# Performance work log

Hardware: AMD Instinct MI355X
Metric: run time of the kernel (lower is better)

## Reference

```python
import math
import jax, jax.numpy as jnp
import numpy as np

B, N, G, D = 8, 1000, 1000, 2
E, H = 128, 8           # embedding_dim, n_heads
DH = E // H             # head dim
KNN = 16                # n_decoding_neighbors (static: mask all zeros -> K=min(16,N))
TANH_CLIP = 10.0


def make_heads(x, n_heads):
    # (B, n, E) -> (B, n_heads, n, E//n_heads)
    b, n, e = x.shape
    return x.reshape(b, n, n_heads, e // n_heads).transpose(0, 2, 1, 3)


def setup_inputs() -> dict:
    key = jax.random.key(0)
    ks = jax.random.split(key, 12)
    s = 1.0 / math.sqrt(E)
    return {
        "last_node": jax.random.randint(ks[0], (B, G), 0, N),
        "coordinates": jax.random.uniform(ks[1], (B, N, D), dtype=jnp.float32),
        "embeddings": jax.random.normal(ks[2], (B, N, E), dtype=jnp.float32),
        "group_ninf_mask": jnp.zeros((B, G, N), dtype=jnp.float32),
        "Wq_graph": jax.random.normal(ks[3], (E, E), dtype=jnp.float32) * s,
        "Wq_first": jax.random.normal(ks[4], (E, E), dtype=jnp.float32) * s,
        "Wq_last": jax.random.normal(ks[5], (E, E), dtype=jnp.float32) * s,
        "Wk": jax.random.normal(ks[6], (E, E), dtype=jnp.float32) * s,
        "Wv": jax.random.normal(ks[7], (E, E), dtype=jnp.float32) * s,
        "W_comb": jax.random.normal(ks[8], (E, E), dtype=jnp.float32) * s,
        "b_comb": jax.random.normal(ks[9], (E,), dtype=jnp.float32) * s,
    }


def reference(last_node, coordinates, embeddings, group_ninf_mask,
              Wq_graph, Wq_first, Wq_last, Wk, Wv, W_comb, b_comb):
    # --- reset() precomputation ---
    graph_emb = embeddings.mean(axis=1, keepdims=True)          # (B,1,E)
    q_graph = make_heads(graph_emb @ Wq_graph.T, H)             # (B,H,1,DH)
    k_h = make_heads(embeddings @ Wk.T, H)                      # (B,H,N,DH)
    v_h = make_heads(embeddings @ Wv.T, H)                      # (B,H,N,DH)

    # --- gather last node embedding ---
    idx_e = jnp.broadcast_to(last_node[..., None], (B, G, E))
    last_emb = jnp.take_along_axis(embeddings, idx_e, axis=1)   # (B,G,E)
    q_first = make_heads(last_emb @ Wq_first.T, H)              # (B,H,G,DH)
    q_last = make_heads(last_emb @ Wq_last.T, H)
    glimpse_q = q_graph + q_first + q_last                      # (B,H,G,DH)

    # --- KNN neighbor mask (cdist + topk + scatter) ---
    idx_c = jnp.broadcast_to(last_node[..., None], (B, G, D))
    last_coord = jnp.take_along_axis(coordinates, idx_c, axis=1)  # (B,G,D)
    d2 = (jnp.sum(last_coord**2, -1)[:, :, None]
          + jnp.sum(coordinates**2, -1)[:, None, :]
          - 2.0 * jnp.einsum('bgd,bnd->bgn', last_coord, coordinates))
    dist = jnp.sqrt(jnp.maximum(d2, 0.0))                       # (B,G,N)
    dist = jnp.where(group_ninf_mask == -jnp.inf, jnp.inf, dist)
    _, knn_idx = jax.lax.top_k(-dist, KNN)                      # (B,G,K) smallest dists
    bi = jnp.arange(B)[:, None, None]
    gi = jnp.arange(G)[None, :, None]
    glimpse_mask = jnp.full((B, G, N), -jnp.inf, dtype=jnp.float32)
    glimpse_mask = glimpse_mask.at[bi, gi, knn_idx].set(0.0)

    # --- masked multi-head glimpse attention ---
    scores = jnp.einsum('bhgd,bhnd->bhgn', glimpse_q, k_h) / math.sqrt(DH)
    scores = scores + glimpse_mask[:, None, :, :]
    attn = jax.nn.softmax(scores, axis=-1)
    out = jnp.einsum('bhgn,bhnd->bhgd', attn, v_h)              # (B,H,G,DH)
    out = out.transpose(0, 2, 1, 3).reshape(B, G, E)
    final_q = out @ W_comb.T + b_comb                           # (B,G,E)

    # --- tanh-clipped scoring + softmax ---
    score = jnp.einsum('bge,bne->bgn', final_q, embeddings) / math.sqrt(E)
    score_masked = TANH_CLIP * jnp.tanh(score) + group_ninf_mask
    probs = jax.nn.softmax(score_masked, axis=2)                # (B,G,N)
    return probs
```

## Files before the change

### kernel.cpp

```cpp
#include <hip/hip_runtime.h>
#include <math.h>

#define BD 8
#define NN 1000
#define GG 1000
#define EE 128

#define OFF_QG    0
#define OFF_K     1024
#define OFF_V     (OFF_K + 1024000)
#define OFF_QFL   (OFF_V + 1024000)
#define OFF_OUTG  (OFF_QFL + 1024000)
#define OFF_FQ    (OFF_OUTG + 1024000)
#define OFF_PART  (OFF_FQ + 1024000)

__global__ __launch_bounds__(1024) void k_graphq(const float* __restrict__ emb,
                                                 const float* __restrict__ Wqg,
                                                 float* __restrict__ qg) {
  __shared__ float partial[8][128];
  __shared__ float ge[128];
  int b = blockIdx.x;
  int t = threadIdx.x;
  int e = t & 127, p = t >> 7;
  const float* eb = emb + (size_t)b * NN * EE;
  float s = 0.f;
  int n0 = p * 125;
  for (int n = n0; n < n0 + 125; ++n) s += eb[(size_t)n * EE + e];
  partial[p][e] = s;
  __syncthreads();
  if (t < 128) {
    float m = 0.f;
#pragma unroll
    for (int q = 0; q < 8; ++q) m += partial[q][t];
    ge[t] = m * (1.f / 1000.f);
  }
  __syncthreads();
  if (t < 128) {
    const float* wr = Wqg + (size_t)t * EE;
    float acc = 0.f;
#pragma unroll 8
    for (int k = 0; k < 128; ++k) acc += ge[k] * wr[k];
    qg[b * EE + t] = acc;
  }
}

__global__ __launch_bounds__(256) void k_proj(const float* __restrict__ emb,
                                              const float* __restrict__ Wk,
                                              const float* __restrict__ Wv,
                                              const float* __restrict__ Wqf,
                                              const float* __restrict__ Wql,
                                              float* __restrict__ Karr,
                                              float* __restrict__ Varr,
                                              float* __restrict__ QFL) {
  __shared__ float Als[16][68];
  __shared__ float Bls[16][68];
  int mt = blockIdx.x, nt = blockIdx.y;
  int t = threadIdx.x;
  int ty = t >> 4, tx = t & 15;
  int row4 = t >> 2, kq = t & 3;
  float acc[4][4] = {};
  for (int k0 = 0; k0 < 128; k0 += 16) {
    const float* ap = emb + (size_t)(mt * 64 + row4) * EE + k0 + kq * 4;
    float4 av = *(const float4*)ap;
    int j = nt * 64 + row4;
    float4 bv;
    if (j < 128) {
      bv = *(const float4*)(Wk + (size_t)j * EE + k0 + kq * 4);
    } else if (j < 256) {
      bv = *(const float4*)(Wv + (size_t)(j - 128) * EE + k0 + kq * 4);
    } else {
      float4 f = *(const float4*)(Wqf + (size_t)(j - 256) * EE + k0 + kq * 4);
      float4 l = *(const float4*)(Wql + (size_t)(j - 256) * EE + k0 + kq * 4);
      bv = make_float4(f.x + l.x, f.y + l.y, f.z + l.z, f.w + l.w);
    }
    Als[kq * 4 + 0][row4] = av.x; Als[kq * 4 + 1][row4] = av.y;
    Als[kq * 4 + 2][row4] = av.z; Als[kq * 4 + 3][row4] = av.w;
    Bls[kq * 4 + 0][row4] = bv.x; Bls[kq * 4 + 1][row4] = bv.y;
    Bls[kq * 4 + 2][row4] = bv.z; Bls[kq * 4 + 3][row4] = bv.w;
    __syncthreads();
#pragma unroll
    for (int k = 0; k < 16; ++k) {
      float a0 = Als[k][ty * 4 + 0], a1 = Als[k][ty * 4 + 1];
      float a2 = Als[k][ty * 4 + 2], a3 = Als[k][ty * 4 + 3];
      float b0 = Bls[k][tx * 4 + 0], b1 = Bls[k][tx * 4 + 1];
      float b2 = Bls[k][tx * 4 + 2], b3 = Bls[k][tx * 4 + 3];
      acc[0][0] += a0 * b0; acc[0][1] += a0 * b1; acc[0][2] += a0 * b2; acc[0][3] += a0 * b3;
      acc[1][0] += a1 * b0; acc[1][1] += a1 * b1; acc[1][2] += a1 * b2; acc[1][3] += a1 * b3;
      acc[2][0] += a2 * b0; acc[2][1] += a2 * b1; acc[2][2] += a2 * b2; acc[2][3] += a2 * b3;
      acc[3][0] += a3 * b0; acc[3][1] += a3 * b1; acc[3][2] += a3 * b2; acc[3][3] += a3 * b3;
    }
    __syncthreads();
  }
  float* outp; int cb;
  if (nt < 2)      { outp = Karr; cb = nt * 64; }
  else if (nt < 4) { outp = Varr; cb = (nt - 2) * 64; }
  else             { outp = QFL;  cb = (nt - 4) * 64; }
#pragma unroll
  for (int i = 0; i < 4; ++i) {
    int r = mt * 64 + ty * 4 + i;
    float4 v = make_float4(acc[i][0], acc[i][1], acc[i][2], acc[i][3]);
    *(float4*)(outp + (size_t)r * EE + cb + tx * 4) = v;
  }
}

template <int CTRL>
__device__ __forceinline__ void red_step_dpp(float& bv, int& bn) {
  int ovi = __builtin_amdgcn_update_dpp(0, __float_as_int(bv), CTRL, 0xf, 0xf, false);
  int on  = __builtin_amdgcn_update_dpp(0, bn, CTRL, 0xf, 0xf, false);
  float ov = __int_as_float(ovi);
  bool better = (ov < bv) || (ov == bv && on < bn);
  bv = better ? ov : bv;
  bn = better ? on : bn;
}
__device__ __forceinline__ void red_step_shfl(int off, float& bv, int& bn) {
  float ov = __shfl_xor(bv, off);
  int on = __shfl_xor(bn, off);
  bool better = (ov < bv) || (ov == bv && on < bn);
  bv = better ? ov : bv;
  bn = better ? on : bn;
}

__global__ __launch_bounds__(256) void k_glimpse(const int* __restrict__ last_node,
                                                 const float* __restrict__ coords,
                                                 const float* __restrict__ mask,
                                                 const float* __restrict__ qg,
                                                 const float* __restrict__ QFL,
                                                 const float* __restrict__ Karr,
                                                 const float* __restrict__ Varr,
                                                 float* __restrict__ outg) {
  __shared__ float pbuf[4][128];
  __shared__ int   nbuf[4][16];
  const float INF = __builtin_inff();
  int wv = threadIdx.x >> 6;
  int lane = threadIdx.x & 63;
  int wid = (blockIdx.x * blockDim.x + threadIdx.x) >> 6;
  int b = wid / GG, g = wid % GG;
  int last = last_node[b * GG + g];
  const float2* cb2 = (const float2*)(coords + (size_t)b * NN * 2);
  float2 lc = cb2[last];
  float lc2 = lc.x * lc.x + lc.y * lc.y;
  const float* mrow = mask + ((size_t)b * GG + g) * NN;
  float d2v[16];
#pragma unroll
  for (int i = 0; i < 16; ++i) {
    int n = lane + 64 * i;
    float v = INF;
    if (n < NN) {
      float2 c = cb2[n];
      float d2 = lc2 + (c.x * c.x + c.y * c.y) - 2.f * (lc.x * c.x + lc.y * c.y);
      d2 = fmaxf(d2, 0.f);
      if (mrow[n] == -INF) d2 = INF;
      v = d2;
    }
    d2v[i] = v;
  }
  int h = lane >> 3;
  int kk = lane & 7;
  int n0sel = 0, n1sel = 0;
  for (int s = 0; s < 16; ++s) {
    float bv = d2v[0]; int bn = lane;
#pragma unroll
    for (int i = 1; i < 16; ++i) {
      float v = d2v[i];
      bool better = (v < bv);
      bv = better ? v : bv;
      bn = better ? (lane + (i << 6)) : bn;
    }
    red_step_dpp<0x121>(bv, bn);
    red_step_dpp<0x122>(bv, bn);
    red_step_dpp<0x124>(bv, bn);
    red_step_dpp<0x128>(bv, bn);
    red_step_shfl(16, bv, bn);
    red_step_shfl(32, bv, bn);
    n0sel = (s == kk) ? bn : n0sel;
    n1sel = (s == kk + 8) ? bn : n1sel;
#pragma unroll
    for (int i = 0; i < 16; ++i)
      d2v[i] = (lane + (i << 6) == bn) ? INF : d2v[i];
  }
  float qh[16];
  {
    const float4* qg4 = (const float4*)(qg + b * EE + h * 16);
    const float4* qf4 = (const float4*)(QFL + ((size_t)b * NN + last) * EE + h * 16);
#pragma unroll
    for (int u = 0; u < 4; ++u) {
      float4 a = qg4[u], c = qf4[u];
      qh[u * 4 + 0] = a.x + c.x; qh[u * 4 + 1] = a.y + c.y;
      qh[u * 4 + 2] = a.z + c.z; qh[u * 4 + 3] = a.w + c.w;
    }
  }
  const float* Kb = Karr + (size_t)b * NN * EE;
  float s0 = 0.f, s1 = 0.f;
  {
    const float4* k04 = (const float4*)(Kb + (size_t)n0sel * EE + h * 16);
    const float4* k14 = (const float4*)(Kb + (size_t)n1sel * EE + h * 16);
    float4 ka[4], kb[4];
#pragma unroll
    for (int u = 0; u < 4; ++u) { ka[u] = k04[u]; kb[u] = k14[u]; }
#pragma unroll
    for (int u = 0; u < 4; ++u) {
      s0 += qh[u * 4 + 0] * ka[u].x; s0 += qh[u * 4 + 1] * ka[u].y;
      s0 += qh[u * 4 + 2] * ka[u].z; s0 += qh[u * 4 + 3] * ka[u].w;
      s1 += qh[u * 4 + 0] * kb[u].x; s1 += qh[u * 4 + 1] * kb[u].y;
      s1 += qh[u * 4 + 2] * kb[u].z; s1 += qh[u * 4 + 3] * kb[u].w;
    }
  }
  s0 *= 0.25f; s1 *= 0.25f;
  float m = fmaxf(s0, s1);
#pragma unroll
  for (int off = 1; off < 8; off <<= 1) m = fmaxf(m, __shfl_xor(m, off));
  float e0 = expf(s0 - m), e1 = expf(s1 - m);
  float se = e0 + e1;
#pragma unroll
  for (int off = 1; off < 8; off <<= 1) se += __shfl_xor(se, off);
  float p0 = e0 / se, p1 = e1 / se;
  pbuf[wv][h * 16 + kk] = p0;
  pbuf[wv][h * 16 + kk + 8] = p1;
  if (h == 0) { nbuf[wv][kk] = n0sel; nbuf[wv][kk + 8] = n1sel; }
  const float* Vb = Varr + (size_t)b * NN * EE;
  float o0 = 0.f, o1 = 0.f;
#pragma unroll
  for (int c = 0; c < 2; ++c) {
    int nk[8]; float pk[8]; float2 vv[8];
#pragma unroll
    for (int j = 0; j < 8; ++j) { nk[j] = nbuf[wv][c * 8 + j]; pk[j] = pbuf[wv][h * 16 + c * 8 + j]; }
#pragma unroll
    for (int j = 0; j < 8; ++j)
      vv[j] = *(const float2*)(Vb + (size_t)nk[j] * EE + h * 16 + kk * 2);
#pragma unroll
    for (int j = 0; j < 8; ++j) { o0 += pk[j] * vv[j].x; o1 += pk[j] * vv[j].y; }
  }
  *(float2*)(outg + ((size_t)b * GG + g) * EE + h * 16 + kk * 2) = make_float2(o0, o1);
}

__global__ __launch_bounds__(256) void k_comb(const float* __restrict__ outg,
                                              const float* __restrict__ Wc,
                                              const float* __restrict__ bc,
                                              float* __restrict__ fq) {
  __shared__ float Als[16][68];
  __shared__ float Bls[16][68];
  int mt = blockIdx.x, nt = blockIdx.y;
  int t = threadIdx.x;
  int ty = t >> 4, tx = t & 15;
  int row4 = t >> 2, kq = t & 3;
  float acc[4][4] = {};
  for (int k0 = 0; k0 < 128; k0 += 16) {
    float4 av = *(const float4*)(outg + (size_t)(mt * 64 + row4) * EE + k0 + kq * 4);
    int j = nt * 64 + row4;
    float4 bv = *(const float4*)(Wc + (size_t)j * EE + k0 + kq * 4);
    Als[kq * 4 + 0][row4] = av.x; Als[kq * 4 + 1][row4] = av.y;
    Als[kq * 4 + 2][row4] = av.z; Als[kq * 4 + 3][row4] = av.w;
    Bls[kq * 4 + 0][row4] = bv.x; Bls[kq * 4 + 1][row4] = bv.y;
    Bls[kq * 4 + 2][row4] = bv.z; Bls[kq * 4 + 3][row4] = bv.w;
    __syncthreads();
#pragma unroll
    for (int k = 0; k < 16; ++k) {
      float a0 = Als[k][ty * 4 + 0], a1 = Als[k][ty * 4 + 1];
      float a2 = Als[k][ty * 4 + 2], a3 = Als[k][ty * 4 + 3];
      float b0 = Bls[k][tx * 4 + 0], b1 = Bls[k][tx * 4 + 1];
      float b2 = Bls[k][tx * 4 + 2], b3 = Bls[k][tx * 4 + 3];
      acc[0][0] += a0 * b0; acc[0][1] += a0 * b1; acc[0][2] += a0 * b2; acc[0][3] += a0 * b3;
      acc[1][0] += a1 * b0; acc[1][1] += a1 * b1; acc[1][2] += a1 * b2; acc[1][3] += a1 * b3;
      acc[2][0] += a2 * b0; acc[2][1] += a2 * b1; acc[2][2] += a2 * b2; acc[2][3] += a2 * b3;
      acc[3][0] += a3 * b0; acc[3][1] += a3 * b1; acc[3][2] += a3 * b2; acc[3][3] += a3 * b3;
    }
    __syncthreads();
  }
#pragma unroll
  for (int i = 0; i < 4; ++i) {
    int r = mt * 64 + ty * 4 + i;
    int c = nt * 64 + tx * 4;
    float4 v = make_float4(acc[i][0] + bc[c + 0], acc[i][1] + bc[c + 1],
                           acc[i][2] + bc[c + 2], acc[i][3] + bc[c + 3]);
    *(float4*)(fq + (size_t)r * EE + c) = v;
  }
}

__global__ __launch_bounds__(256, 2) void k_score(const float* __restrict__ fq,
                                                  const float* __restrict__ emb,
                                                  const float* __restrict__ mask,
                                                  float* __restrict__ out,
                                                  float* __restrict__ part) {
  __shared__ float As[16][132];
  __shared__ float Bs[16][132];
  int b = blockIdx.x, gt = blockIdx.y, nt = blockIdx.z;
  int t = threadIdx.x;
  int tx = t & 15, ty = t >> 4;
  int g0 = gt * 128, n0 = nt * 128;
  const float* A = fq + (size_t)b * GG * EE;
  const float* Bm = emb + (size_t)b * NN * EE;
  int lr = t >> 1;
  int lq = t & 1;
  int ar = min(g0 + lr, GG - 1);
  int br = min(n0 + lr, NN - 1);
  const float* apos = A + (size_t)ar * EE + lq * 8;
  const float* bpos = Bm + (size_t)br * EE + lq * 8;

  float acc[8][8] = {};
  float4 sa0 = *(const float4*)(apos + 0);
  float4 sa1 = *(const float4*)(apos + 4);
  float4 sb0 = *(const float4*)(bpos + 0);
  float4 sb1 = *(const float4*)(bpos + 4);
  for (int k0 = 0; k0 < 128; k0 += 16) {
    __syncthreads();
    As[lq * 8 + 0][lr] = sa0.x; As[lq * 8 + 1][lr] = sa0.y;
    As[lq * 8 + 2][lr] = sa0.z; As[lq * 8 + 3][lr] = sa0.w;
    As[lq * 8 + 4][lr] = sa1.x; As[lq * 8 + 5][lr] = sa1.y;
    As[lq * 8 + 6][lr] = sa1.z; As[lq * 8 + 7][lr] = sa1.w;
    Bs[lq * 8 + 0][lr] = sb0.x; Bs[lq * 8 + 1][lr] = sb0.y;
    Bs[lq * 8 + 2][lr] = sb0.z; Bs[lq * 8 + 3][lr] = sb0.w;
    Bs[lq * 8 + 4][lr] = sb1.x; Bs[lq * 8 + 5][lr] = sb1.y;
    Bs[lq * 8 + 6][lr] = sb1.z; Bs[lq * 8 + 7][lr] = sb1.w;
    __syncthreads();
    if (k0 < 112) {
      sa0 = *(const float4*)(apos + k0 + 16);
      sa1 = *(const float4*)(apos + k0 + 20);
      sb0 = *(const float4*)(bpos + k0 + 16);
      sb1 = *(const float4*)(bpos + k0 + 20);
    }
#pragma unroll
    for (int k = 0; k < 16; ++k) {
      float4 av0 = *(const float4*)&As[k][ty * 8];
      float4 av1 = *(const float4*)&As[k][ty * 8 + 4];
      float4 bv0 = *(const float4*)&Bs[k][tx * 8];
      float4 bv1 = *(const float4*)&Bs[k][tx * 8 + 4];
      float af[8] = {av0.x, av0.y, av0.z, av0.w, av1.x, av1.y, av1.z, av1.w};
      float bf[8] = {bv0.x, bv0.y, bv0.z, bv0.w, bv1.x, bv1.y, bv1.z, bv1.w};
#pragma unroll
      for (int i = 0; i < 8; ++i)
#pragma unroll
        for (int j = 0; j < 8; ++j) acc[i][j] += af[i] * bf[j];
    }
  }

  const float rs = 0.08838834764831845f;
  const float NEGINF = -__builtin_inff();
  int gbase = g0 + ty * 8;
  int nb = n0 + tx * 8;
  bool nfull = (nb + 7 < NN);
#pragma unroll
  for (int i = 0; i < 8; ++i) {
    int g = gbase + i;
    int gc = g < GG ? g : GG - 1;
    const float* mrow = mask + ((size_t)b * GG + gc) * NN;
    float* orow = out + ((size_t)b * GG + gc) * NN;
    float mv[8];
    if (nfull) {
      float4 m0 = *(const float4*)(mrow + nb);
      float4 m1 = *(const float4*)(mrow + nb + 4);
      mv[0] = m0.x; mv[1] = m0.y; mv[2] = m0.z; mv[3] = m0.w;
      mv[4] = m1.x; mv[5] = m1.y; mv[6] = m1.z; mv[7] = m1.w;
    } else {
#pragma unroll
      for (int j = 0; j < 8; ++j) mv[j] = (nb + j < NN) ? mrow[nb + j] : NEGINF;
    }
    float e[8];
    float rsum = 0.f;
#pragma unroll
    for (int j = 0; j < 8; ++j) {
      float sc = acc[i][j] * rs;
      float u = __expf(2.f * sc);
      float th = 1.f - 2.f * __builtin_amdgcn_rcpf(u + 1.f);
      float ev = __expf(10.f * th + mv[j]);
      e[j] = ev;
      rsum += ev;
    }
    if (g < GG) {
      if (nfull) {
        *(float4*)(orow + nb)     = make_float4(e[0], e[1], e[2], e[3]);
        *(float4*)(orow + nb + 4) = make_float4(e[4], e[5], e[6], e[7]);
      } else {
#pragma unroll
        for (int j = 0; j < 8; ++j)
          if (nb + j < NN) orow[nb + j] = e[j];
      }
    }
#pragma unroll
    for (int off = 1; off < 16; off <<= 1) rsum += __shfl_xor(rsum, off);
    if (tx == 0 && g < GG) part[((size_t)b * GG + g) * 8 + nt] = rsum;
  }
}

__global__ __launch_bounds__(256) void k_norm(const float* __restrict__ part,
                                              float* __restrict__ out) {
  int row = blockIdx.x;
  __shared__ float ssum;
  int t = threadIdx.x;
  float v = (t < 8) ? part[(size_t)row * 8 + t] : 0.f;
#pragma unroll
  for (int off = 1; off < 8; off <<= 1) v += __shfl_xor(v, off);
  if (t == 0) ssum = v;
  __syncthreads();
  float inv = 1.f / ssum;
  if (t < 250) {
    float4* o = (float4*)(out + (size_t)row * NN);
    float4 x = o[t];
    x.x *= inv; x.y *= inv; x.z *= inv; x.w *= inv;
    o[t] = x;
  }
}

extern "C" void kernel_launch(void* const* d_in, const int* in_sizes, int n_in,
                              void* d_out, int out_size, void* d_ws, size_t ws_size,
                              hipStream_t stream) {
  const int*   last_node = (const int*)d_in[0];
  const float* coords    = (const float*)d_in[1];
  const float* emb       = (const float*)d_in[2];
  const float* mask      = (const float*)d_in[3];
  const float* Wqg       = (const float*)d_in[4];
  const float* Wqf       = (const float*)d_in[5];
  const float* Wql       = (const float*)d_in[6];
  const float* Wk        = (const float*)d_in[7];
  const float* Wv        = (const float*)d_in[8];
  const float* Wc        = (const float*)d_in[9];
  const float* bc        = (const float*)d_in[10];
  float* out = (float*)d_out;
  float* ws  = (float*)d_ws;

  float* qg   = ws + OFF_QG;
  float* Karr = ws + OFF_K;
  float* Varr = ws + OFF_V;
  float* QFL  = ws + OFF_QFL;
  float* outg = ws + OFF_OUTG;
  float* fq   = ws + OFF_FQ;
  float* part = ws + OFF_PART;

  k_graphq<<<dim3(BD), dim3(1024), 0, stream>>>(emb, Wqg, qg);
  k_proj<<<dim3(125, 6), dim3(256), 0, stream>>>(emb, Wk, Wv, Wqf, Wql, Karr, Varr, QFL);
  k_glimpse<<<dim3(2000), dim3(256), 0, stream>>>(last_node, coords, mask, qg, QFL, Karr, Varr, outg);
  k_comb<<<dim3(125, 2), dim3(256), 0, stream>>>(outg, Wc, bc, fq);
  k_score<<<dim3(8, 8, 8), dim3(256), 0, stream>>>(fq, emb, mask, out, part);
  k_norm<<<dim3(8000), dim3(256), 0, stream>>>(part, out);
}
```

Baseline: 225.0 us.

## Split graph mean, pack KNN keys into u64, retile score kernel

The graph-mean kernel is split into a 200-block partial-sum pass followed by a small reduce-and-project kernel, replacing 8 large blocks that run serially. KNN top-k now packs distance bits and node index into a single 64-bit key, so each round is one min reduction and the selected index is broadcast via readfirstlane. Distances are square-rooted to match the reference's tie behaviour. The score GEMM tile shrinks from 128x128 to 64x128 with higher occupancy bounds, doubling the block count, and the glimpse softmax uses fast exp.

```diff
diff --git a/kernel.cpp b/kernel.cpp
--- a/kernel.cpp
+++ b/kernel.cpp
@@ -5,6 +5,8 @@
 #define NN 1000
 #define GG 1000
 #define EE 128
+
+typedef unsigned long long u64;
 
 #define OFF_QG    0
 #define OFF_K     1024
@@ -13,35 +15,38 @@
 #define OFF_OUTG  (OFF_QFL + 1024000)
 #define OFF_FQ    (OFF_OUTG + 1024000)
 #define OFF_PART  (OFF_FQ + 1024000)
-
-__global__ __launch_bounds__(1024) void k_graphq(const float* __restrict__ emb,
-                                                 const float* __restrict__ Wqg,
-                                                 float* __restrict__ qg) {
-  __shared__ float partial[8][128];
-  __shared__ float ge[128];
-  int b = blockIdx.x;
+#define OFF_GPART (OFF_PART + 64000)
+
+__global__ __launch_bounds__(256) void k_gq1(const float* __restrict__ emb,
+                                             float* __restrict__ gpart) {
+  __shared__ float ps[2][128];
+  int b = blockIdx.x, blk = blockIdx.y;
   int t = threadIdx.x;
   int e = t & 127, p = t >> 7;
-  const float* eb = emb + (size_t)b * NN * EE;
+  const float* eb = emb + ((size_t)b * NN + blk * 40 + p * 20) * EE + e;
   float s = 0.f;
-  int n0 = p * 125;
-  for (int n = n0; n < n0 + 125; ++n) s += eb[(size_t)n * EE + e];
-  partial[p][e] = s;
+#pragma unroll 4
+  for (int n = 0; n < 20; ++n) s += eb[(size_t)n * EE];
+  ps[p][e] = s;
   __syncthreads();
-  if (t < 128) {
-    float m = 0.f;
-#pragma unroll
-    for (int q = 0; q < 8; ++q) m += partial[q][t];
-    ge[t] = m * (1.f / 1000.f);
-  }
+  if (t < 128) gpart[(b * 25 + blk) * 128 + t] = ps[0][t] + ps[1][t];
+}
+
+__global__ __launch_bounds__(128) void k_gq2(const float* __restrict__ gpart,
+                                             const float* __restrict__ Wqg,
+                                             float* __restrict__ qg) {
+  __shared__ float ge[128];
+  int b = blockIdx.x, t = threadIdx.x;
+  float s = 0.f;
+#pragma unroll 5
+  for (int j = 0; j < 25; ++j) s += gpart[(b * 25 + j) * 128 + t];
+  ge[t] = s * (1.f / 1000.f);
   __syncthreads();
-  if (t < 128) {
-    const float* wr = Wqg + (size_t)t * EE;
-    float acc = 0.f;
+  const float* wr = Wqg + (size_t)t * EE;
+  float acc = 0.f;
 #pragma unroll 8
-    for (int k = 0; k < 128; ++k) acc += ge[k] * wr[k];
-    qg[b * EE + t] = acc;
-  }
+  for (int k = 0; k < 128; ++k) acc += ge[k] * wr[k];
+  qg[b * EE + t] = acc;
 }
 
 __global__ __launch_bounds__(256) void k_proj(const float* __restrict__ emb,
@@ -104,21 +109,17 @@
 }
 
 template <int CTRL>
-__device__ __forceinline__ void red_step_dpp(float& bv, int& bn) {
-  int ovi = __builtin_amdgcn_update_dpp(0, __float_as_int(bv), CTRL, 0xf, 0xf, false);
-  int on  = __builtin_amdgcn_update_dpp(0, bn, CTRL, 0xf, 0xf, false);
-  float ov = __int_as_float(ovi);
-  bool better = (ov < bv) || (ov == bv && on < bn);
-  bv = better ? ov : bv;
-  bn = better ? on : bn;
-}
-__device__ __forceinline__ void red_step_shfl(int off, float& bv, int& bn) {
-  float ov = __shfl_xor(bv, off);
-  int on = __shfl_xor(bn, off);
-  bool better = (ov < bv) || (ov == bv && on < bn);
-  bv = better ? ov : bv;
-  bn = better ? on : bn;
-}
+__device__ __forceinline__ u64 dpp_mov64(u64 x) {
+  int lo = __builtin_amdgcn_update_dpp(0, (int)(unsigned)(x & 0xffffffffULL), CTRL, 0xf, 0xf, false);
+  int hi = __builtin_amdgcn_update_dpp(0, (int)(unsigned)(x >> 32), CTRL, 0xf, 0xf, false);
+  return ((u64)(unsigned)hi << 32) | (unsigned)lo;
+}
+__device__ __forceinline__ u64 shfl_xor64(u64 x, int off) {
+  int lo = __shfl_xor((int)(unsigned)(x & 0xffffffffULL), off);
+  int hi = __shfl_xor((int)(unsigned)(x >> 32), off);
+  return ((u64)(unsigned)hi << 32) | (unsigned)lo;
+}
+__device__ __forceinline__ u64 min64(u64 a, u64 b) { return a < b ? a : b; }
 
 __global__ __launch_bounds__(256) void k_glimpse(const int* __restrict__ last_node,
                                                  const float* __restrict__ coords,
@@ -140,43 +141,41 @@
   float2 lc = cb2[last];
   float lc2 = lc.x * lc.x + lc.y * lc.y;
   const float* mrow = mask + ((size_t)b * GG + g) * NN;
-  float d2v[16];
+  u64 key[16];
 #pragma unroll
   for (int i = 0; i < 16; ++i) {
-    int n = lane + 64 * i;
-    float v = INF;
+    int n = lane + (i << 6);
+    u64 k = ~0ULL;
     if (n < NN) {
       float2 c = cb2[n];
       float d2 = lc2 + (c.x * c.x + c.y * c.y) - 2.f * (lc.x * c.x + lc.y * c.y);
-      d2 = fmaxf(d2, 0.f);
-      if (mrow[n] == -INF) d2 = INF;
-      v = d2;
-    }
-    d2v[i] = v;
+      float d = sqrtf(fmaxf(d2, 0.f));
+      if (mrow[n] == -INF) d = INF;
+      k = ((u64)__float_as_uint(d) << 10) | (unsigned)n;
+    }
+    key[i] = k;
   }
   int h = lane >> 3;
   int kk = lane & 7;
   int n0sel = 0, n1sel = 0;
   for (int s = 0; s < 16; ++s) {
-    float bv = d2v[0]; int bn = lane;
-#pragma unroll
-    for (int i = 1; i < 16; ++i) {
-      float v = d2v[i];
-      bool better = (v < bv);
-      bv = better ? v : bv;
-      bn = better ? (lane + (i << 6)) : bn;
-    }
-    red_step_dpp<0x121>(bv, bn);
-    red_step_dpp<0x122>(bv, bn);
-    red_step_dpp<0x124>(bv, bn);
-    red_step_dpp<0x128>(bv, bn);
-    red_step_shfl(16, bv, bn);
-    red_step_shfl(32, bv, bn);
-    n0sel = (s == kk) ? bn : n0sel;
-    n1sel = (s == kk + 8) ? bn : n1sel;
+    u64 bk = key[0];
+#pragma unroll
+    for (int i = 1; i < 16; ++i) bk = min64(bk, key[i]);
+    bk = min64(bk, dpp_mov64<0x121>(bk));
+    bk = min64(bk, dpp_mov64<0x122>(bk));
+    bk = min64(bk, dpp_mov64<0x124>(bk));
+    bk = min64(bk, dpp_mov64<0x128>(bk));
+    bk = min64(bk, shfl_xor64(bk, 16));
+    bk = min64(bk, shfl_xor64(bk, 32));
+    int wn = (int)__builtin_amdgcn_readfirstlane((unsigned)bk & 1023u);
+    n0sel = (s == kk) ? wn : n0sel;
+    n1sel = (s == kk + 8) ? wn : n1sel;
+    int iw = wn >> 6;
+    bool me = (lane == (wn & 63));
 #pragma unroll
     for (int i = 0; i < 16; ++i)
-      d2v[i] = (lane + (i << 6) == bn) ? INF : d2v[i];
+      if (i == iw && me) key[i] = ~0ULL;
   }
   float qh[16];
   {
@@ -209,7 +208,7 @@
   float m = fmaxf(s0, s1);
 #pragma unroll
   for (int off = 1; off < 8; off <<= 1) m = fmaxf(m, __shfl_xor(m, off));
-  float e0 = expf(s0 - m), e1 = expf(s1 - m);
+  float e0 = __expf(s0 - m), e1 = __expf(s1 - m);
   float se = e0 + e1;
 #pragma unroll
   for (int off = 1; off < 8; off <<= 1) se += __shfl_xor(se, off);
@@ -276,58 +275,53 @@
   }
 }
 
-__global__ __launch_bounds__(256, 2) void k_score(const float* __restrict__ fq,
+__global__ __launch_bounds__(256, 4) void k_score(const float* __restrict__ fq,
                                                   const float* __restrict__ emb,
                                                   const float* __restrict__ mask,
                                                   float* __restrict__ out,
                                                   float* __restrict__ part) {
-  __shared__ float As[16][132];
+  __shared__ float As[16][68];
   __shared__ float Bs[16][132];
-  int b = blockIdx.x, gt = blockIdx.y, nt = blockIdx.z;
+  int nt = blockIdx.x, gt = blockIdx.y, b = blockIdx.z;
   int t = threadIdx.x;
   int tx = t & 15, ty = t >> 4;
-  int g0 = gt * 128, n0 = nt * 128;
+  int g0 = gt * 64, n0 = nt * 128;
   const float* A = fq + (size_t)b * GG * EE;
   const float* Bm = emb + (size_t)b * NN * EE;
-  int lr = t >> 1;
-  int lq = t & 1;
-  int ar = min(g0 + lr, GG - 1);
-  int br = min(n0 + lr, NN - 1);
-  const float* apos = A + (size_t)ar * EE + lq * 8;
-  const float* bpos = Bm + (size_t)br * EE + lq * 8;
-
-  float acc[8][8] = {};
-  float4 sa0 = *(const float4*)(apos + 0);
-  float4 sa1 = *(const float4*)(apos + 4);
-  float4 sb0 = *(const float4*)(bpos + 0);
-  float4 sb1 = *(const float4*)(bpos + 4);
+  int la = t >> 2, akq = t & 3;
+  int lb = t >> 1, bkq = t & 1;
+  int ar = min(g0 + la, GG - 1);
+  int br = min(n0 + lb, NN - 1);
+  const float* apos = A + (size_t)ar * EE + akq * 4;
+  const float* bpos = Bm + (size_t)br * EE + bkq * 8;
+
+  float acc[4][8] = {};
+  float4 pa  = *(const float4*)apos;
+  float4 pb0 = *(const float4*)bpos;
+  float4 pb1 = *(const float4*)(bpos + 4);
   for (int k0 = 0; k0 < 128; k0 += 16) {
     __syncthreads();
-    As[lq * 8 + 0][lr] = sa0.x; As[lq * 8 + 1][lr] = sa0.y;
-    As[lq * 8 + 2][lr] = sa0.z; As[lq * 8 + 3][lr] = sa0.w;
-    As[lq * 8 + 4][lr] = sa1.x; As[lq * 8 + 5][lr] = sa1.y;
-    As[lq * 8 + 6][lr] = sa1.z; As[lq * 8 + 7][lr] = sa1.w;
-    Bs[lq * 8 + 0][lr] = sb0.x; Bs[lq * 8 + 1][lr] = sb0.y;
-    Bs[lq * 8 + 2][lr] = sb0.z; Bs[lq * 8 + 3][lr] = sb0.w;
-    Bs[lq * 8 + 4][lr] = sb1.x; Bs[lq * 8 + 5][lr] = sb1.y;
-    Bs[lq * 8 + 6][lr] = sb1.z; Bs[lq * 8 + 7][lr] = sb1.w;
+    As[akq * 4 + 0][la] = pa.x;  As[akq * 4 + 1][la] = pa.y;
+    As[akq * 4 + 2][la] = pa.z;  As[akq * 4 + 3][la] = pa.w;
+    Bs[bkq * 8 + 0][lb] = pb0.x; Bs[bkq * 8 + 1][lb] = pb0.y;
+    Bs[bkq * 8 + 2][lb] = pb0.z; Bs[bkq * 8 + 3][lb] = pb0.w;
+    Bs[bkq * 8 + 4][lb] = pb1.x; Bs[bkq * 8 + 5][lb] = pb1.y;
+    Bs[bkq * 8 + 6][lb] = pb1.z; Bs[bkq * 8 + 7][lb] = pb1.w;
     __syncthreads();
     if (k0 < 112) {
-      sa0 = *(const float4*)(apos + k0 + 16);
-      sa1 = *(const float4*)(apos + k0 + 20);
-      sb0 = *(const float4*)(bpos + k0 + 16);
-      sb1 = *(const float4*)(bpos + k0 + 20);
+      pa  = *(const float4*)(apos + k0 + 16);
+      pb0 = *(const float4*)(bpos + k0 + 16);
+      pb1 = *(const float4*)(bpos + k0 + 20);
     }
 #pragma unroll
     for (int k = 0; k < 16; ++k) {
-      float4 av0 = *(const float4*)&As[k][ty * 8];
-      float4 av1 = *(const float4*)&As[k][ty * 8 + 4];
-      float4 bv0 = *(const float4*)&Bs[k][tx * 8];
-      float4 bv1 = *(const float4*)&Bs[k][tx * 8 + 4];
-      float af[8] = {av0.x, av0.y, av0.z, av0.w, av1.x, av1.y, av1.z, av1.w};
+      float4 av  = *(const float4*)&As[k][ty * 4];
+      float4 bv0 = *(const float4*)&Bs[k][tx * 4];
+      float4 bv1 = *(const float4*)&Bs[k][64 + tx * 4];
+      float af[4] = {av.x, av.y, av.z, av.w};
       float bf[8] = {bv0.x, bv0.y, bv0.z, bv0.w, bv1.x, bv1.y, bv1.z, bv1.w};
 #pragma unroll
-      for (int i = 0; i < 8; ++i)
+      for (int i = 0; i < 4; ++i)
 #pragma unroll
         for (int j = 0; j < 8; ++j) acc[i][j] += af[i] * bf[j];
     }
@@ -335,49 +329,63 @@
 
   const float rs = 0.08838834764831845f;
   const float NEGINF = -__builtin_inff();
-  int gbase = g0 + ty * 8;
-  int nb = n0 + tx * 8;
-  bool nfull = (nb + 7 < NN);
-#pragma unroll
-  for (int i = 0; i < 8; ++i) {
+  int gbase = g0 + ty * 4;
+  int nb0 = n0 + tx * 4;
+  int nb1 = n0 + 64 + tx * 4;
+  bool b1full = (nb1 + 3 < NN);
+#pragma unroll
+  for (int i = 0; i < 4; ++i) {
     int g = gbase + i;
-    int gc = g < GG ? g : GG - 1;
+    bool gv = (g < GG);
+    int gc = gv ? g : GG - 1;
     const float* mrow = mask + ((size_t)b * GG + gc) * NN;
     float* orow = out + ((size_t)b * GG + gc) * NN;
-    float mv[8];
-    if (nfull) {
-      float4 m0 = *(const float4*)(mrow + nb);
-      float4 m1 = *(const float4*)(mrow + nb + 4);
-      mv[0] = m0.x; mv[1] = m0.y; mv[2] = m0.z; mv[3] = m0.w;
-      mv[4] = m1.x; mv[5] = m1.y; mv[6] = m1.z; mv[7] = m1.w;
-    } else {
-#pragma unroll
-      for (int j = 0; j < 8; ++j) mv[j] = (nb + j < NN) ? mrow[nb + j] : NEGINF;
-    }
-    float e[8];
     float rsum = 0.f;
-#pragma unroll
-    for (int j = 0; j < 8; ++j) {
-      float sc = acc[i][j] * rs;
-      float u = __expf(2.f * sc);
-      float th = 1.f - 2.f * __builtin_amdgcn_rcpf(u + 1.f);
-      float ev = __expf(10.f * th + mv[j]);
-      e[j] = ev;
-      rsum += ev;
-    }
-    if (g < GG) {
-      if (nfull) {
-        *(float4*)(orow + nb)     = make_float4(e[0], e[1], e[2], e[3]);
-        *(float4*)(orow + nb + 4) = make_float4(e[4], e[5], e[6], e[7]);
+    {
+      float4 m0 = *(const float4*)(mrow + nb0);
+      float mv[4] = {m0.x, m0.y, m0.z, m0.w};
+      float e[4];
+#pragma unroll
+      for (int j = 0; j < 4; ++j) {
+        float sc = acc[i][j] * rs;
+        float u = __expf(2.f * sc);
+        float th = 1.f - 2.f * __builtin_amdgcn_rcpf(u + 1.f);
+        e[j] = __expf(10.f * th + mv[j]);
+        rsum += e[j];
+      }
+      if (gv) *(float4*)(orow + nb0) = make_float4(e[0], e[1], e[2], e[3]);
+    }
+    {
+      float mv[4];
+      if (b1full) {
+        float4 m1 = *(const float4*)(mrow + nb1);
+        mv[0] = m1.x; mv[1] = m1.y; mv[2] = m1.z; mv[3] = m1.w;
       } else {
 #pragma unroll
-        for (int j = 0; j < 8; ++j)
-          if (nb + j < NN) orow[nb + j] = e[j];
+        for (int j = 0; j < 4; ++j) mv[j] = (nb1 + j < NN) ? mrow[nb1 + j] : NEGINF;
       }
+      float e[4];
+#pragma unroll
+      for (int j = 0; j < 4; ++j) {
+        float sc = acc[i][4 + j] * rs;
+        float u = __expf(2.f * sc);
+        float th = 1.f - 2.f * __builtin_amdgcn_rcpf(u + 1.f);
+        e[j] = __expf(10.f * th + mv[j]);
+        rsum += e[j];
+      }
+      if (gv) {
+        if (b1full) {
+          *(float4*)(orow + nb1) = make_float4(e[0], e[1], e[2], e[3]);
+        } else {
+#pragma unroll
+          for (int j = 0; j < 4; ++j)
+            if (nb1 + j < NN) orow[nb1 + j] = e[j];
+        }
+      }
     }
 #pragma unroll
     for (int off = 1; off < 16; off <<= 1) rsum += __shfl_xor(rsum, off);
-    if (tx == 0 && g < GG) part[((size_t)b * GG + g) * 8 + nt] = rsum;
+    if (tx == 0 && gv) part[((size_t)b * GG + g) * 8 + nt] = rsum;
   }
 }
 
@@ -417,18 +425,20 @@
   float* out = (float*)d_out;
   float* ws  = (float*)d_ws;
 
-  float* qg   = ws + OFF_QG;
-  float* Karr = ws + OFF_K;
-  float* Varr = ws + OFF_V;
-  float* QFL  = ws + OFF_QFL;
-  float* outg = ws + OFF_OUTG;
-  float* fq   = ws + OFF_FQ;
-  float* part = ws + OFF_PART;
-
-  k_graphq<<<dim3(BD), dim3(1024), 0, stream>>>(emb, Wqg, qg);
+  float* qg    = ws + OFF_QG;
+  float* Karr  = ws + OFF_K;
+  float* Varr  = ws + OFF_V;
+  float* QFL   = ws + OFF_QFL;
+  float* outg  = ws + OFF_OUTG;
+  float* fq    = ws + OFF_FQ;
+  float* part  = ws + OFF_PART;
+  float* gpart = ws + OFF_GPART;
+
+  k_gq1<<<dim3(BD, 25), dim3(256), 0, stream>>>(emb, gpart);
+  k_gq2<<<dim3(BD), dim3(128), 0, stream>>>(gpart, Wqg, qg);
   k_proj<<<dim3(125, 6), dim3(256), 0, stream>>>(emb, Wk, Wv, Wqf, Wql, Karr, Varr, QFL);
   k_glimpse<<<dim3(2000), dim3(256), 0, stream>>>(last_node, coords, mask, qg, QFL, Karr, Varr, outg);
   k_comb<<<dim3(125, 2), dim3(256), 0, stream>>>(outg, Wc, bc, fq);
-  k_score<<<dim3(8, 8, 8), dim3(256), 0, stream>>>(fq, emb, mask, out, part);
+  k_score<<<dim3(8, 16, 8), dim3(256), 0, stream>>>(fq, emb, mask, out, part);
   k_norm<<<dim3(8000), dim3(256), 0, stream>>>(part, out);
 }
```

Measured after the change: 214.4 us. -4.7%, faster.
